# Performance work log

Measured on AMD Instinct MI355X. Metric: run time of the kernel, lower is better.

## Reference

```python
import jax, jax.numpy as jnp
import numpy as np

B, N, F, FE, H, C = 2, 2048, 128, 8, 4, 64
LEAKY_ALPHA = 0.2
NEG_INF = -1e9


def setup_inputs() -> dict:
    key = jax.random.key(0)
    ks = jax.random.split(key, 8)
    return {
        "X": jax.random.normal(ks[0], (B, N, F), jnp.float32),
        "A": jax.random.uniform(ks[1], (B, N, N), jnp.float32),
        "E": jax.random.normal(ks[2], (B, N, N, FE), jnp.float32),
        "W_edge": jax.random.normal(ks[3], (FE, 1), jnp.float32) * 0.1,
        "b_edge": jnp.zeros((1,), jnp.float32),
        "W_gat": jax.random.normal(ks[4], (H, F, C), jnp.float32) * 0.05,
        "a_src": jax.random.normal(ks[5], (H, C), jnp.float32) * 0.1,
        "a_dst": jax.random.normal(ks[6], (H, C), jnp.float32) * 0.1,
        "b_gat": jnp.zeros((H * C,), jnp.float32),
        "ln_gamma": jnp.ones((H * C,), jnp.float32),
        "ln_beta": jnp.zeros((H * C,), jnp.float32),
    }


def reference(X, A, E, W_edge, b_edge, W_gat, a_src, a_dst, b_gat, ln_gamma, ln_beta):
    # --- edge gate: sigmoid(Dense_1(E)) -> [B,N,N], multiply into adjacency ---
    edge_w = jax.nn.sigmoid(jnp.einsum("bije,eo->bijo", E, W_edge) + b_edge)
    A = A * edge_w[..., 0]  # [B,N,N]

    # --- multi-head dense GAT (spektral GATConv, concat_heads, elu) ---
    h = jnp.einsum("bnf,hfc->bnhc", X, W_gat)  # [B,N,H,C]
    s_src = jnp.einsum("bnhc,hc->bnh", h, a_src)  # [B,N,H]
    s_dst = jnp.einsum("bnhc,hc->bnh", h, a_dst)
    # e_ij = LeakyReLU(src_i + dst_j): [B,N(i),N(j),H]
    logits = jax.nn.leaky_relu(s_src[:, :, None, :] + s_dst[:, None, :, :],
                               negative_slope=LEAKY_ALPHA)
    mask = jnp.where(A == 0.0, NEG_INF, 0.0)[..., None]  # [B,N,N,1]
    attn = jax.nn.softmax(logits + mask, axis=2)  # softmax over neighbors j
    out = jnp.einsum("bijh,bjhc->bihc", attn, h)  # [B,N,H,C]
    out = out.reshape(B, N, H * C) + b_gat
    out = jax.nn.elu(out)

    # --- LayerNorm over the feature axis (inference: dropout is identity) ---
    mu = jnp.mean(out, axis=-1, keepdims=True)
    var = jnp.var(out, axis=-1, keepdims=True)
    out = (out - mu) * jax.lax.rsqrt(var + 1e-3) * ln_gamma + ln_beta
    return out
```

## Files before the change

kernel.cpp:

```cpp
#include <hip/hip_runtime.h>
#include <hip/hip_bf16.h>


#define BB 2
#define NN 2048
#define FF 128
#define HH 4
#define CC 64
#define HC 256
#define TN 8
#define LOG2E 1.4426950408889634f

typedef __attribute__((ext_vector_type(8))) short short8;
typedef __attribute__((ext_vector_type(4))) float f32x4;

__device__ __forceinline__ float wave_sum(float v) {
#pragma unroll
    for (int m = 32; m >= 1; m >>= 1) v += __shfl_xor(v, m, 64);
    return v;
}

__device__ __forceinline__ unsigned short bf16rne(float x) {
    unsigned u = __float_as_uint(x);
    return (unsigned short)((u + 0x7fffu + ((u >> 16) & 1u)) >> 16);
}

__global__ __launch_bounds__(256) void k1_proj(
    const float* __restrict__ X, const float* __restrict__ Wg,
    const float* __restrict__ a_src, const float* __restrict__ a_dst,
    unsigned short* __restrict__ hT, float* __restrict__ ssT,
    float* __restrict__ sdT)
{
    __shared__ float sX[TN][FF];
    const int blk = blockIdx.x;
    const int b  = blk / (NN / TN);
    const int n0 = (blk % (NN / TN)) * TN;
    const int tid = threadIdx.x;
    const int h = tid >> 6, c = tid & 63;

    for (int idx = tid; idx < TN * FF; idx += 256) {
        int r = idx >> 7, f = idx & 127;
        sX[r][f] = X[(size_t)(b * NN + n0 + r) * FF + f];
    }
    __syncthreads();

    float hv[TN];
#pragma unroll
    for (int r = 0; r < TN; ++r) hv[r] = 0.f;

#pragma unroll 4
    for (int f4 = 0; f4 < FF / 4; ++f4) {
        const int f = f4 * 4;
        const float w0 = Wg[(h * FF + f + 0) * CC + c];
        const float w1 = Wg[(h * FF + f + 1) * CC + c];
        const float w2 = Wg[(h * FF + f + 2) * CC + c];
        const float w3 = Wg[(h * FF + f + 3) * CC + c];
#pragma unroll
        for (int r = 0; r < TN; ++r) {
            float4 x4 = *(const float4*)&sX[r][f];
            hv[r] = fmaf(x4.x, w0, hv[r]);
            hv[r] = fmaf(x4.y, w1, hv[r]);
            hv[r] = fmaf(x4.z, w2, hv[r]);
            hv[r] = fmaf(x4.w, w3, hv[r]);
        }
    }

    union { short8 v; unsigned short u[8]; } pk;
#pragma unroll
    for (int r = 0; r < TN; ++r) pk.u[r] = bf16rne(hv[r]);
    *(short8*)&hT[((size_t)(b * HH + h) * CC + c) * NN + n0] = pk.v;

    const float as = a_src[tid];
    const float ad = a_dst[tid];
#pragma unroll
    for (int r = 0; r < TN; ++r) {
        const int n = n0 + r;
        float s1 = wave_sum(hv[r] * as);
        float s2 = wave_sum(hv[r] * ad);
        if (c == 0) {
            ssT[(b * HH + h) * NN + n] = s1 * LOG2E;
            sdT[(b * HH + h) * NN + n] = s2 * LOG2E;
        }
    }
}

struct Stage {
    float4 aa, ab;
    float4 sda, sdb;
    short8 bfr[4];
};

__device__ __forceinline__ void load_stage(
    Stage& s, const float* adjp, const float* sdp,
    const unsigned short* const* hb, int js)
{
    s.aa  = *(const float4*)(adjp + js);
    s.ab  = *(const float4*)(adjp + js + 4);
    s.sda = *(const float4*)(sdp + js);
    s.sdb = *(const float4*)(sdp + js + 4);
#pragma unroll
    for (int ni = 0; ni < 4; ++ni) s.bfr[ni] = *(const short8*)(hb[ni] + js);
}

__device__ __forceinline__ void consume_stage(
    const Stage& s, float ss, float& lsum, f32x4* acc)
{
    const float sd[8] = {s.sda.x, s.sda.y, s.sda.z, s.sda.w,
                         s.sdb.x, s.sdb.y, s.sdb.z, s.sdb.w};
    const float av[8] = {s.aa.x, s.aa.y, s.aa.z, s.aa.w,
                         s.ab.x, s.ab.y, s.ab.z, s.ab.w};
    float p[8];
#pragma unroll
    for (int t = 0; t < 8; ++t) {
        float x = ss + sd[t];
        x = fmaxf(x, 0.2f * x);
        float pv = (av[t] == 0.f) ? 0.f : __builtin_amdgcn_exp2f(x);
        lsum += pv;
        p[t] = pv;
    }
    union { short8 v; __hip_bfloat162 h2[4]; } pk;
#pragma unroll
    for (int t = 0; t < 4; ++t)
        pk.h2[t] = __float22bfloat162_rn(make_float2(p[2 * t], p[2 * t + 1]));
#pragma unroll
    for (int ni = 0; ni < 4; ++ni)
        acc[ni] = __builtin_amdgcn_mfma_f32_16x16x32_bf16(pk.v, s.bfr[ni], acc[ni], 0, 0, 0);
}

__global__ __launch_bounds__(1024) void k2_attn(
    const float* __restrict__ Adj, const unsigned short* __restrict__ hT,
    const float* __restrict__ ssT, const float* __restrict__ sdT,
    const float* __restrict__ b_gat, const float* __restrict__ gamma,
    const float* __restrict__ beta, float* __restrict__ out)
{
    __shared__ float accs[3][16][HH][64];
    __shared__ float lsumx[3][HH][16];
    __shared__ float red1s[HH][16], red2s[HH][16];

    const int blk = blockIdx.x;
    const int b  = blk >> 7;
    const int i0 = (blk & 127) << 4;
    const int tid  = threadIdx.x;
    const int wave = tid >> 6;
    const int h  = wave & 3;
    const int jq = wave >> 2;
    const int l  = tid & 63;
    const int lr = l & 15;
    const int lq = l >> 4;

    const float ss = ssT[(b * HH + h) * NN + i0 + lr];

    f32x4 acc[4];
#pragma unroll
    for (int ni = 0; ni < 4; ++ni) acc[ni] = (f32x4){0.f, 0.f, 0.f, 0.f};
    float lsum = 0.f;

    const float* adjp = Adj + (size_t)(b * NN + i0 + lr) * NN + jq * 512 + lq * 8;
    const float* sdp  = sdT + (b * HH + h) * NN + jq * 512 + lq * 8;
    const unsigned short* hb[4];
#pragma unroll
    for (int ni = 0; ni < 4; ++ni)
        hb[ni] = hT + ((size_t)(b * HH + h) * CC + ni * 16 + lr) * NN + jq * 512 + lq * 8;

    Stage s0, s1;
    load_stage(s0, adjp, sdp, hb, 0);
#pragma unroll 2
    for (int it = 0; it < 16; it += 2) {
        load_stage(s1, adjp, sdp, hb, (it + 1) * 32);
        consume_stage(s0, ss, lsum, acc);
        if (it + 2 < 16) load_stage(s0, adjp, sdp, hb, (it + 2) * 32);
        consume_stage(s1, ss, lsum, acc);
    }

    lsum += __shfl_xor(lsum, 16, 64);
    lsum += __shfl_xor(lsum, 32, 64);

    if (jq > 0) {
        if (lq == 0) lsumx[jq - 1][h][lr] = lsum;
#pragma unroll
        for (int ni = 0; ni < 4; ++ni)
#pragma unroll
            for (int r = 0; r < 4; ++r)
                accs[jq - 1][ni * 4 + r][h][l] = acc[ni][r];
    }
    __syncthreads();

    if (jq == 0) {
        const float lcomb = lsum + lsumx[0][h][lr] + lsumx[1][h][lr] + lsumx[2][h][lr];
        float lrow[4];
#pragma unroll
        for (int r = 0; r < 4; ++r) lrow[r] = __shfl(lcomb, lq * 4 + r, 64);

        float bg[4];
#pragma unroll
        for (int ni = 0; ni < 4; ++ni) bg[ni] = b_gat[h * 64 + ni * 16 + lr];

        float vals[4][4];
        float s1[4] = {0.f, 0.f, 0.f, 0.f}, s2[4] = {0.f, 0.f, 0.f, 0.f};
#pragma unroll
        for (int ni = 0; ni < 4; ++ni)
#pragma unroll
            for (int r = 0; r < 4; ++r) {
                float a = acc[ni][r] + accs[0][ni * 4 + r][h][l]
                        + accs[1][ni * 4 + r][h][l] + accs[2][ni * 4 + r][h][l];
                float v = a / lrow[r] + bg[ni];
                v = (v > 0.f) ? v : (__expf(v) - 1.f);
                vals[ni][r] = v;
                s1[r] += v;
                s2[r] += v * v;
            }
#pragma unroll
        for (int m = 1; m <= 8; m <<= 1)
#pragma unroll
            for (int r = 0; r < 4; ++r) {
                s1[r] += __shfl_xor(s1[r], m, 64);
                s2[r] += __shfl_xor(s2[r], m, 64);
            }
        if (lr == 0)
#pragma unroll
            for (int r = 0; r < 4; ++r) {
                red1s[h][lq * 4 + r] = s1[r];
                red2s[h][lq * 4 + r] = s2[r];
            }
        __syncthreads();

        const float gm[4] = {gamma[h * 64 + lr], gamma[h * 64 + 16 + lr],
                             gamma[h * 64 + 32 + lr], gamma[h * 64 + 48 + lr]};
        const float bm[4] = {beta[h * 64 + lr], beta[h * 64 + 16 + lr],
                             beta[h * 64 + 32 + lr], beta[h * 64 + 48 + lr]};
#pragma unroll
        for (int r = 0; r < 4; ++r) {
            const int row = lq * 4 + r;
            float S1 = red1s[0][row] + red1s[1][row] + red1s[2][row] + red1s[3][row];
            float S2 = red2s[0][row] + red2s[1][row] + red2s[2][row] + red2s[3][row];
            float mu  = S1 * (1.f / HC);
            float var = S2 * (1.f / HC) - mu * mu;
            float inv = rsqrtf(var + 1e-3f);
            float* op = out + (size_t)(b * NN + i0 + row) * HC + h * 64 + lr;
#pragma unroll
            for (int ni = 0; ni < 4; ++ni)
                op[ni * 16] = (vals[ni][r] - mu) * inv * gm[ni] + bm[ni];
        }
    } else {
        __syncthreads();
    }
}

extern "C" void kernel_launch(void* const* d_in, const int* in_sizes, int n_in,
                              void* d_out, int out_size, void* d_ws, size_t ws_size,
                              hipStream_t stream)
{
    const float* X     = (const float*)d_in[0];
    const float* Adj   = (const float*)d_in[1];
    const float* Wg    = (const float*)d_in[5];
    const float* a_src = (const float*)d_in[6];
    const float* a_dst = (const float*)d_in[7];
    const float* b_gat = (const float*)d_in[8];
    const float* gam   = (const float*)d_in[9];
    const float* bet   = (const float*)d_in[10];
    float* out = (float*)d_out;

    const size_t hT_elems = (size_t)BB * HH * CC * NN;
    const size_t ss_elems = (size_t)BB * HH * NN;

    unsigned short* hT = (unsigned short*)d_ws;
    float* ssT = (float*)(hT + hT_elems);
    float* sdT = ssT + ss_elems;

    k1_proj<<<BB * NN / TN, 256, 0, stream>>>(X, Wg, a_src, a_dst, hT, ssT, sdT);
    k2_attn<<<BB * (NN / 16), 1024, 0, stream>>>(Adj, hT, ssT, sdT, b_gat, gam, bet, out);
}
```

Baseline: 387.0 us.

## Precompute adjacency zero-mask bitfield in projection kernel, drop Adj reads from attention

The projection kernel now also scans the fp32 adjacency and writes a per-row bitmask of zero entries, laid out to match the attention kernel's lane/iteration order. The attention kernel loads one uint4 of mask bits per lane instead of streaming fp32 adjacency values in its pipelined inner loop, and only applies masking when bits are set. This shrinks the attention kernel's per-stage loads and register use, but moves the full adjacency read into the first kernel and adds scattered byte writes.

```diff
diff --git a/kernel.cpp b/kernel.cpp
--- a/kernel.cpp
+++ b/kernel.cpp
@@ -26,10 +26,11 @@
 }
 
 __global__ __launch_bounds__(256) void k1_proj(
-    const float* __restrict__ X, const float* __restrict__ Wg,
+    const float* __restrict__ X, const float* __restrict__ Adj,
+    const float* __restrict__ Wg,
     const float* __restrict__ a_src, const float* __restrict__ a_dst,
     unsigned short* __restrict__ hT, float* __restrict__ ssT,
-    float* __restrict__ sdT)
+    float* __restrict__ sdT, unsigned char* __restrict__ zT)
 {
     __shared__ float sX[TN][FF];
     const int blk = blockIdx.x;
@@ -82,20 +83,42 @@
             sdT[(b * HH + h) * NN + n] = s2 * LOG2E;
         }
     }
+
+    {
+        const int r = tid >> 5;
+        const int s = tid & 31;
+        const size_t row = (size_t)(b * NN + n0 + r);
+        const float* ap = Adj + row * NN + s * 64;
+        unsigned char* zp = zT + (row << 8);
+#pragma unroll
+        for (int k = 0; k < 8; ++k) {
+            float4 a0 = *(const float4*)(ap + k * 8);
+            float4 a1 = *(const float4*)(ap + k * 8 + 4);
+            unsigned m = 0u;
+            m |= (a0.x == 0.f) ? 1u   : 0u;
+            m |= (a0.y == 0.f) ? 2u   : 0u;
+            m |= (a0.z == 0.f) ? 4u   : 0u;
+            m |= (a0.w == 0.f) ? 8u   : 0u;
+            m |= (a1.x == 0.f) ? 16u  : 0u;
+            m |= (a1.y == 0.f) ? 32u  : 0u;
+            m |= (a1.z == 0.f) ? 64u  : 0u;
+            m |= (a1.w == 0.f) ? 128u : 0u;
+            const int jb = s * 8 + k;
+            const int jq = jb >> 6, rem = jb & 63;
+            const int it = rem >> 2, lq = rem & 3;
+            zp[jq * 64 + lq * 16 + it] = (unsigned char)m;
+        }
+    }
 }
 
 struct Stage {
-    float4 aa, ab;
     float4 sda, sdb;
     short8 bfr[4];
 };
 
 __device__ __forceinline__ void load_stage(
-    Stage& s, const float* adjp, const float* sdp,
-    const unsigned short* const* hb, int js)
-{
-    s.aa  = *(const float4*)(adjp + js);
-    s.ab  = *(const float4*)(adjp + js + 4);
+    Stage& s, const float* sdp, const unsigned short* const* hb, int js)
+{
     s.sda = *(const float4*)(sdp + js);
     s.sdb = *(const float4*)(sdp + js + 4);
 #pragma unroll
@@ -103,21 +126,25 @@
 }
 
 __device__ __forceinline__ void consume_stage(
-    const Stage& s, float ss, float& lsum, f32x4* acc)
+    const Stage& s, float ss, unsigned mb, float& lsum, f32x4* acc)
 {
     const float sd[8] = {s.sda.x, s.sda.y, s.sda.z, s.sda.w,
                          s.sdb.x, s.sdb.y, s.sdb.z, s.sdb.w};
-    const float av[8] = {s.aa.x, s.aa.y, s.aa.z, s.aa.w,
-                         s.ab.x, s.ab.y, s.ab.z, s.ab.w};
     float p[8];
 #pragma unroll
     for (int t = 0; t < 8; ++t) {
         float x = ss + sd[t];
         x = fmaxf(x, 0.2f * x);
-        float pv = (av[t] == 0.f) ? 0.f : __builtin_amdgcn_exp2f(x);
-        lsum += pv;
-        p[t] = pv;
-    }
+        p[t] = __builtin_amdgcn_exp2f(x);
+    }
+    if (mb) {
+#pragma unroll
+        for (int t = 0; t < 8; ++t)
+            if ((mb >> t) & 1u) p[t] = 0.f;
+    }
+#pragma unroll
+    for (int t = 0; t < 8; ++t) lsum += p[t];
+
     union { short8 v; __hip_bfloat162 h2[4]; } pk;
 #pragma unroll
     for (int t = 0; t < 4; ++t)
@@ -128,8 +155,8 @@
 }
 
 __global__ __launch_bounds__(1024) void k2_attn(
-    const float* __restrict__ Adj, const unsigned short* __restrict__ hT,
-    const float* __restrict__ ssT, const float* __restrict__ sdT,
+    const unsigned short* __restrict__ hT, const float* __restrict__ ssT,
+    const float* __restrict__ sdT, const unsigned char* __restrict__ zT,
     const float* __restrict__ b_gat, const float* __restrict__ gamma,
     const float* __restrict__ beta, float* __restrict__ out)
 {
@@ -150,12 +177,14 @@
 
     const float ss = ssT[(b * HH + h) * NN + i0 + lr];
 
+    const uint4 mw = *(const uint4*)(zT + ((size_t)(b * NN + i0 + lr) << 8)
+                                       + jq * 64 + lq * 16);
+
     f32x4 acc[4];
 #pragma unroll
     for (int ni = 0; ni < 4; ++ni) acc[ni] = (f32x4){0.f, 0.f, 0.f, 0.f};
     float lsum = 0.f;
 
-    const float* adjp = Adj + (size_t)(b * NN + i0 + lr) * NN + jq * 512 + lq * 8;
     const float* sdp  = sdT + (b * HH + h) * NN + jq * 512 + lq * 8;
     const unsigned short* hb[4];
 #pragma unroll
@@ -163,13 +192,19 @@
         hb[ni] = hT + ((size_t)(b * HH + h) * CC + ni * 16 + lr) * NN + jq * 512 + lq * 8;
 
     Stage s0, s1;
-    load_stage(s0, adjp, sdp, hb, 0);
-#pragma unroll 2
-    for (int it = 0; it < 16; it += 2) {
-        load_stage(s1, adjp, sdp, hb, (it + 1) * 32);
-        consume_stage(s0, ss, lsum, acc);
-        if (it + 2 < 16) load_stage(s0, adjp, sdp, hb, (it + 2) * 32);
-        consume_stage(s1, ss, lsum, acc);
+    load_stage(s0, sdp, hb, 0);
+#pragma unroll
+    for (int w = 0; w < 4; ++w) {
+        const unsigned mword = (w == 0) ? mw.x : (w == 1) ? mw.y
+                             : (w == 2) ? mw.z : mw.w;
+#pragma unroll
+        for (int k = 0; k < 4; k += 2) {
+            const int it = w * 4 + k;
+            load_stage(s1, sdp, hb, (it + 1) * 32);
+            consume_stage(s0, ss, (mword >> (k * 8)) & 0xffu, lsum, acc);
+            if (it + 2 < 16) load_stage(s0, sdp, hb, (it + 2) * 32);
+            consume_stage(s1, ss, (mword >> ((k + 1) * 8)) & 0xffu, lsum, acc);
+        }
     }
 
     lsum += __shfl_xor(lsum, 16, 64);
@@ -266,7 +301,8 @@
     unsigned short* hT = (unsigned short*)d_ws;
     float* ssT = (float*)(hT + hT_elems);
     float* sdT = ssT + ss_elems;
-
-    k1_proj<<<BB * NN / TN, 256, 0, stream>>>(X, Wg, a_src, a_dst, hT, ssT, sdT);
-    k2_attn<<<BB * (NN / 16), 1024, 0, stream>>>(Adj, hT, ssT, sdT, b_gat, gam, bet, out);
-}
+    unsigned char* zT = (unsigned char*)(sdT + ss_elems);
+
+    k1_proj<<<BB * NN / TN, 256, 0, stream>>>(X, Adj, Wg, a_src, a_dst, hT, ssT, sdT, zT);
+    k2_attn<<<BB * (NN / 16), 1024, 0, stream>>>(hT, ssT, sdT, zT, b_gat, gam, bet, out);
+}
```

After: 615.5 us. 1.59x slower.
